# Kernel tuning notes

Measured on AMD Instinct MI355X. Metric: run time of the kernel, lower is better.

Reference implementation:

```python
import jax, jax.numpy as jnp
import numpy as np

DIM = 128
NUM_LAYERS = 2
N_LEGO = 50000
N_POINT = 100000
E_LL = 500000
E_PP = 400000
E_LP = 500000
E_PL = 500000


def _seg_softmax(score, seg, n):
    m = jax.ops.segment_max(score, seg, num_segments=n)
    m = jnp.where(jnp.isfinite(m), m, 0.0)
    e = jnp.exp(score - m[seg])
    d = jax.ops.segment_sum(e, seg, num_segments=n)
    return e / (d[seg] + 1e-16)


def _trans_conv(xs, xd, src, dst, Wq, bq, Wk, bk, Wv, bv, Ws, bs):
    # PyG TransformerConv, heads=1, root skip, no edge features
    q = xd @ Wq + bq
    k = xs @ Wk + bk
    v = xs @ Wv + bv
    score = (q[dst] * k[src]).sum(-1) / jnp.sqrt(jnp.asarray(DIM, q.dtype))
    a = _seg_softmax(score, dst, xd.shape[0])
    agg = jax.ops.segment_sum(a[:, None] * v[src], dst, num_segments=xd.shape[0])
    return agg + xd @ Ws + bs


def _gat_conv(xs, xd, src, dst, W, a_src, a_dst, b):
    # PyG GATConv, heads=1, add_self_loops=False, shared lin for src/dst
    hs = xs @ W
    hd = xd @ W
    score = jax.nn.leaky_relu((hs @ a_src)[src] + (hd @ a_dst)[dst], 0.2)
    a = _seg_softmax(score, dst, xd.shape[0])
    return jax.ops.segment_sum(a[:, None] * hs[src], dst, num_segments=xd.shape[0]) + b


def _edge_conv(x, src, dst, W1, b1, W2, b2):
    # PyG EdgeConv: max_j MLP([x_i, x_j - x_i]); BN treated as identity (eval)
    xi = x[dst]
    h = jax.nn.relu(jnp.concatenate([xi, x[src] - xi], axis=-1) @ W1 + b1)
    m = h @ W2 + b2
    agg = jax.ops.segment_max(m, dst, num_segments=x.shape[0])
    return jnp.where(jnp.isfinite(agg), agg, 0.0)


def _forward(x_lego, x_point, tWq, tbq, tWk, tbk, tWv, tbv, tWs, tbs,
             eW1, eb1, eW2, eb2, gW, gAs, gAd, gb,
             ll_src, ll_dst, pp_src, pp_dst, lp_src, lp_dst, pl_src, pl_dst):
    for layer in range(NUM_LAYERS):
        iA = 2 * layer        # first HeteroConv in the stack
        iB = 2 * layer + 1    # second HeteroConv
        i_lp = 2 * layer      # GAT lego->point instance
        i_pl = 2 * layer + 1  # GAT point->lego instance
        # conv A: 4 relations, HeteroConv sum-aggregation per dst type
        lego_a = _trans_conv(x_lego, x_lego, ll_src, ll_dst,
                             tWq[iA], tbq[iA], tWk[iA], tbk[iA], tWv[iA], tbv[iA], tWs[iA], tbs[iA]) \
               + _gat_conv(x_point, x_lego, pl_src, pl_dst, gW[i_pl], gAs[i_pl], gAd[i_pl], gb[i_pl])
        point_a = _edge_conv(x_point, pp_src, pp_dst, eW1[iA], eb1[iA], eW2[iA], eb2[iA]) \
                + _gat_conv(x_lego, x_point, lp_src, lp_dst, gW[i_lp], gAs[i_lp], gAd[i_lp], gb[i_lp])
        # conv B: intra-type relations only
        x_lego = _trans_conv(lego_a, lego_a, ll_src, ll_dst,
                             tWq[iB], tbq[iB], tWk[iB], tbk[iB], tWv[iB], tbv[iB], tWs[iB], tbs[iB])
        x_point = _edge_conv(point_a, pp_src, pp_dst, eW1[iB], eb1[iB], eW2[iB], eb2[iB])
    return x_lego, x_point


def setup_inputs() -> dict:
    key = jax.random.key(0)
    ks = jax.random.split(key, 32)
    NT = 2 * NUM_LAYERS  # conv instances per conv type
    s = np.float32(1.0 / np.sqrt(DIM))
    sh = np.float32(1.0 / np.sqrt(4 * DIM))
    return {
        "x_lego": jax.random.normal(ks[0], (N_LEGO, DIM), jnp.float32),
        "x_point": jax.random.normal(ks[1], (N_POINT, DIM), jnp.float32),
        "tWq": jax.random.normal(ks[2], (NT, DIM, DIM), jnp.float32) * s,
        "tbq": jnp.zeros((NT, DIM), jnp.float32),
        "tWk": jax.random.normal(ks[3], (NT, DIM, DIM), jnp.float32) * s,
        "tbk": jnp.zeros((NT, DIM), jnp.float32),
        "tWv": jax.random.normal(ks[4], (NT, DIM, DIM), jnp.float32) * s,
        "tbv": jnp.zeros((NT, DIM), jnp.float32),
        "tWs": jax.random.normal(ks[5], (NT, DIM, DIM), jnp.float32) * s,
        "tbs": jnp.zeros((NT, DIM), jnp.float32),
        "eW1": jax.random.normal(ks[6], (NT, 2 * DIM, 4 * DIM), jnp.float32) * s,
        "eb1": jnp.zeros((NT, 4 * DIM), jnp.float32),
        "eW2": jax.random.normal(ks[7], (NT, 4 * DIM, DIM), jnp.float32) * sh,
        "eb2": jnp.zeros((NT, DIM), jnp.float32),
        "gW": jax.random.normal(ks[8], (NT, DIM, DIM), jnp.float32) * s,
        "gAs": jax.random.normal(ks[9], (NT, DIM), jnp.float32) * s,
        "gAd": jax.random.normal(ks[10], (NT, DIM), jnp.float32) * s,
        "gb": jnp.zeros((NT, DIM), jnp.float32),
        "ll_src": jax.random.randint(ks[11], (E_LL,), 0, N_LEGO),
        "ll_dst": jax.random.randint(ks[12], (E_LL,), 0, N_LEGO),
        "pp_src": jax.random.randint(ks[13], (E_PP,), 0, N_POINT),
        "pp_dst": jax.random.randint(ks[14], (E_PP,), 0, N_POINT),
        "lp_src": jax.random.randint(ks[15], (E_LP,), 0, N_LEGO),
        "lp_dst": jax.random.randint(ks[16], (E_LP,), 0, N_POINT),
        "pl_src": jax.random.randint(ks[17], (E_PL,), 0, N_POINT),
        "pl_dst": jax.random.randint(ks[18], (E_PL,), 0, N_LEGO),
    }


def reference(x_lego, x_point, tWq, tbq, tWk, tbk, tWv, tbv, tWs, tbs,
              eW1, eb1, eW2, eb2, gW, gAs, gAd, gb,
              ll_src, ll_dst, pp_src, pp_dst, lp_src, lp_dst, pl_src, pl_dst):
    return _forward(x_lego, x_point, tWq, tbq, tWk, tbk, tWv, tbv, tWs, tbs,
                    eW1, eb1, eW2, eb2, gW, gAs, gAd, gb,
                    ll_src, ll_dst, pp_src, pp_dst, lp_src, lp_dst, pl_src, pl_dst)
```

## Files before the change

### kernel.cpp

```cpp
#include <hip/hip_runtime.h>


typedef unsigned int u32;
typedef unsigned short u16;

#define NL 50000
#define NP 100000
#define ELL 500000
#define EPPE 400000
#define ELPE 500000
#define EPLE 500000
#define ENC_NEG_INF 0x007FFFFFu

using bf16x8 = __attribute__((ext_vector_type(8))) short;
using f32x4  = __attribute__((ext_vector_type(4))) float;
using u16x4  = __attribute__((ext_vector_type(4))) unsigned short;

__device__ __forceinline__ float bf2f(u16 h) { return __uint_as_float(((u32)h) << 16); }
__device__ __forceinline__ u16 f2bf(float f) {
    u32 u = __float_as_uint(f);
    u += 0x7FFFu + ((u >> 16) & 1u);
    return (u16)(u >> 16);
}
__device__ __forceinline__ u32 encf(float f) {
    u32 u = __float_as_uint(f);
    return (u & 0x80000000u) ? ~u : (u | 0x80000000u);
}
__device__ __forceinline__ float decf(u32 u) {
    return __uint_as_float((u & 0x80000000u) ? (u ^ 0x80000000u) : ~u);
}

__global__ void k_detect(const u32* __restrict__ x, u32* __restrict__ flag) {
    int lane = threadIdx.x;
    u16 lo = (u16)(x[lane] & 0xFFFFu);
    float a = fabsf(bf2f(lo));
    int inband = (a > 1e-4f && a < 100.f) ? 1 : 0;
    unsigned long long m = __ballot(inband);
    if (lane == 0) flag[0] = (__popcll(m) >= 32) ? 1u : 0u;
}


__global__ __launch_bounds__(256) void k_cast_any(const void* __restrict__ in,
                                                  float* __restrict__ out, int n,
                                                  const u32* __restrict__ flag) {
    int i = blockIdx.x * 256 + threadIdx.x;
    if (i >= n) return;
    if (flag[0]) out[i] = bf2f(((const u16*)in)[i]);
    else         out[i] = ((const float*)in)[i];
}

__global__ __launch_bounds__(256) void k_store_out(const float* __restrict__ in,
                                                   void* __restrict__ out, size_t off, int n,
                                                   const u32* __restrict__ flag) {
    int i = blockIdx.x * 256 + threadIdx.x;
    if (i >= n) return;
    if (flag[0]) ((u16*)out)[off + i] = f2bf(in[i]);
    else         ((float*)out)[off + i] = in[i];
}

__global__ __launch_bounds__(256) void k_fill_u32(u32* __restrict__ p, u32 v, int n) {
    int i = blockIdx.x * 256 + threadIdx.x;
    if (i < n) p[i] = v;
}

__global__ void k_add128(const float* __restrict__ a, const float* __restrict__ b,
                         float* __restrict__ o) {
    int t = threadIdx.x;
    o[t] = a[t] + b[t];
}

__global__ __launch_bounds__(256) void k_tcast(const float* __restrict__ in,
                                               u16* __restrict__ out,
                                               int K, int N, int total) {
    int i = blockIdx.x * 256 + threadIdx.x;
    if (i >= total) return;
    int per = K * N;
    int c = i / per, r = i - c * per;
    int k = r / N, n = r - k * N;
    out[(size_t)c * per + (size_t)n * K + k] = f2bf(in[i]);
}

__global__ __launch_bounds__(256) void k_w1mod(float* __restrict__ w, int total) {
    int i = blockIdx.x * 256 + threadIdx.x;
    if (i >= total) return;
    int c = i >> 16;
    int r = (i >> 9) & 127;
    int col = i & 511;
    float* base = w + c * 131072;
    base[r * 512 + col] -= base[(r + 128) * 512 + col];
}

__global__ __launch_bounds__(256) void k_split(const float4* __restrict__ x,
                                               u16x4* __restrict__ xh,
                                               u16x4* __restrict__ xl, int n4) {
    int i = blockIdx.x * 256 + threadIdx.x;
    if (i >= n4) return;
    float4 f = x[i];
    float fv[4] = {f.x, f.y, f.z, f.w};
    u16x4 h, l;
#pragma unroll
    for (int j = 0; j < 4; ++j) {
        u16 hi = f2bf(fv[j]);
        h[j] = hi;
        l[j] = f2bf(fv[j] - bf2f(hi));
    }
    xh[i] = h; xl[i] = l;
}

__global__ void k_matvec2(const float* __restrict__ W, const float* __restrict__ a0,
                          const float* __restrict__ a1, float* __restrict__ o) {
    __shared__ float as[128];
    const float* a = blockIdx.x ? a1 : a0;
    int t = threadIdx.x;
    as[t] = a[t];
    __syncthreads();
    float s = 0.f;
#pragma unroll 8
    for (int i = 0; i < 128; ++i) s += W[t * 128 + i] * as[i];
    o[blockIdx.x * 128 + t] = s;
}

__global__ __launch_bounds__(256) void k_node_scalar(const float* __restrict__ X,
                                                     const float* __restrict__ wv,
                                                     float* __restrict__ s, int n) {
    int wid = (blockIdx.x * 256 + threadIdx.x) >> 6;
    int lane = threadIdx.x & 63;
    if (wid >= n) return;
    const float* xr = X + (size_t)wid * 128;
    float v = xr[lane] * wv[lane] + xr[lane + 64] * wv[lane + 64];
#pragma unroll
    for (int o = 32; o; o >>= 1) v += __shfl_xor(v, o);
    if (lane == 0) s[wid] = v;
}


__global__ __launch_bounds__(256) void k_deg(const int* __restrict__ dst,
                                             int* __restrict__ deg, int E) {
    int i = blockIdx.x * 256 + threadIdx.x;
    if (i < E) atomicAdd(deg + dst[i], 1);
}

__global__ __launch_bounds__(256) void k_scan1(const int* __restrict__ deg,
                                               int* __restrict__ rp,
                                               int* __restrict__ aux, int n) {
    __shared__ int ls[256];
    int t = threadIdx.x;
    int i = blockIdx.x * 256 + t;
    int v = (i < n) ? deg[i] : 0;
    ls[t] = v;
    __syncthreads();
#pragma unroll
    for (int off = 1; off < 256; off <<= 1) {
        int a = (t >= off) ? ls[t - off] : 0;
        __syncthreads();
        ls[t] += a;
        __syncthreads();
    }
    if (i < n) rp[i] = ls[t] - v;
    if (t == 255) aux[blockIdx.x] = ls[255];
}

__global__ __launch_bounds__(512) void k_scan2(int* __restrict__ aux, int nb) {
    __shared__ int ls[512];
    int t = threadIdx.x;
    int v = (t < nb) ? aux[t] : 0;
    ls[t] = v;
    __syncthreads();
#pragma unroll
    for (int off = 1; off < 512; off <<= 1) {
        int a = (t >= off) ? ls[t - off] : 0;
        __syncthreads();
        ls[t] += a;
        __syncthreads();
    }
    if (t < nb) aux[t] = ls[t] - v;
}

__global__ __launch_bounds__(256) void k_scan3(int* __restrict__ rp,
                                               const int* __restrict__ aux,
                                               int n, int E) {
    int i = blockIdx.x * 256 + threadIdx.x;
    if (i > n) return;
    if (i == n) rp[n] = E;
    else        rp[i] += aux[i >> 8];
}

__global__ __launch_bounds__(256) void k_copy_i32(const int* __restrict__ a,
                                                  int* __restrict__ b, int n) {
    int i = blockIdx.x * 256 + threadIdx.x;
    if (i < n) b[i] = a[i];
}

__global__ __launch_bounds__(256) void k_scat(const int* __restrict__ src,
                                              const int* __restrict__ dst,
                                              int* __restrict__ cur,
                                              int* __restrict__ col, int E) {
    int i = blockIdx.x * 256 + threadIdx.x;
    if (i >= E) return;
    int pos = atomicAdd(cur + dst[i], 1);
    col[pos] = src[i];
}


__global__ __launch_bounds__(256) void k_attn_trans(const float* __restrict__ Tq,
                                                    const float* __restrict__ Tk,
                                                    const float* __restrict__ Tv,
                                                    const int* __restrict__ rp,
                                                    const int* __restrict__ col,
                                                    float* __restrict__ out, int nd) {
    int row = (blockIdx.x * 256 + threadIdx.x) >> 6;
    int lane = threadIdx.x & 63;
    if (row >= nd) return;
    int e0 = rp[row], e1 = rp[row + 1];
    if (e0 >= e1) return;
    const float* q = Tq + (size_t)row * 128;
    float q0 = q[lane], q1 = q[lane + 64];
    float m = -3.0e38f, l = 0.f, o0 = 0.f, o1 = 0.f;
    for (int e = e0; e < e1; ++e) {
        int s = col[e];
        const float* kr = Tk + (size_t)s * 128;
        float d = q0 * kr[lane] + q1 * kr[lane + 64];
#pragma unroll
        for (int off = 32; off; off >>= 1) d += __shfl_xor(d, off);
        d *= 0.08838834764831845f;
        float mn = fmaxf(m, d);
        float al = expf(m - mn);
        float p  = expf(d - mn);
        const float* vr = Tv + (size_t)s * 128;
        l  = l * al + p;
        o0 = o0 * al + p * vr[lane];
        o1 = o1 * al + p * vr[lane + 64];
        m = mn;
    }
    float inv = 1.f / (l + 1e-16f);
    size_t base = (size_t)row * 128;
    out[base + lane]      += o0 * inv;
    out[base + lane + 64] += o1 * inv;
}

__global__ __launch_bounds__(256) void k_attn_gat(const float* __restrict__ hs,
                                                  const float* __restrict__ ss,
                                                  const float* __restrict__ sd,
                                                  const int* __restrict__ rp,
                                                  const int* __restrict__ col,
                                                  float* __restrict__ out, int nd) {
    int row = (blockIdx.x * 256 + threadIdx.x) >> 6;
    int lane = threadIdx.x & 63;
    if (row >= nd) return;
    int e0 = rp[row], e1 = rp[row + 1];
    if (e0 >= e1) return;
    float sdv = sd[row];
    float m = -3.0e38f, l = 0.f, o0 = 0.f, o1 = 0.f;
    for (int e = e0; e < e1; ++e) {
        int s = col[e];
        float sc = ss[s] + sdv;
        sc = sc > 0.f ? sc : 0.2f * sc;
        float mn = fmaxf(m, sc);
        float al = expf(m - mn);
        float p  = expf(sc - mn);
        const float* hr = hs + (size_t)s * 128;
        l  = l * al + p;
        o0 = o0 * al + p * hr[lane];
        o1 = o1 * al + p * hr[lane + 64];
        m = mn;
    }
    float inv = 1.f / (l + 1e-16f);
    size_t base = (size_t)row * 128;
    out[base + lane]      += o0 * inv;
    out[base + lane + 64] += o1 * inv;
}

#define LSTR 40

__global__ __launch_bounds__(256) void k_mgemm(const float* __restrict__ A_,
                                               const u16* __restrict__ Wt,
                                               const float* __restrict__ bias,
                                               float* __restrict__ Cout,
                                               int M, int N, int K) {
    __shared__ u16 Ahs[128 * LSTR];
    __shared__ u16 Als[128 * LSTR];
    __shared__ u16 Bss[128 * LSTR];
    const int tid = threadIdx.x;
    const int m0 = blockIdx.y * 128, n0 = blockIdx.x * 128;

    const int srow = tid >> 1, sseg = (tid & 1) * 16;
    int arow = m0 + srow;
    if (arow >= M) arow = M - 1;
    const float* Af = A_ + (size_t)arow * K + sseg;
    u16* AhW = &Ahs[srow * LSTR + sseg];
    u16* AlW = &Als[srow * LSTR + sseg];
    const u16* Bp = Wt + (size_t)(n0 + srow) * K + sseg;
    u16* BsW = &Bss[srow * LSTR + sseg];

    const int lane = tid & 63, wv = tid >> 6;
    const int mw = (wv >> 1) * 64, nw = (wv & 1) * 64;
    const int fm = lane & 15, fq = lane >> 4;
    const u16* aRh = &Ahs[(mw + fm) * LSTR + fq * 8];
    const u16* aRl = &Als[(mw + fm) * LSTR + fq * 8];
    const u16* bR  = &Bss[(nw + fm) * LSTR + fq * 8];

    f32x4 acc[4][4];
#pragma unroll
    for (int i = 0; i < 4; ++i)
#pragma unroll
        for (int j = 0; j < 4; ++j) { acc[i][j][0]=0.f; acc[i][j][1]=0.f; acc[i][j][2]=0.f; acc[i][j][3]=0.f; }

    for (int k0 = 0; k0 < K; k0 += 32) {
        __syncthreads();
        float4 f0 = *(const float4*)(Af + k0);
        float4 f1 = *(const float4*)(Af + k0 + 4);
        float4 f2 = *(const float4*)(Af + k0 + 8);
        float4 f3 = *(const float4*)(Af + k0 + 12);
        float v[16] = {f0.x,f0.y,f0.z,f0.w, f1.x,f1.y,f1.z,f1.w,
                       f2.x,f2.y,f2.z,f2.w, f3.x,f3.y,f3.z,f3.w};
        u32 hp[8], lp[8];
#pragma unroll
        for (int i = 0; i < 8; ++i) {
            float x0 = v[2 * i], x1 = v[2 * i + 1];
            u16 h0 = f2bf(x0), h1 = f2bf(x1);
            u16 l0 = f2bf(x0 - bf2f(h0)), l1 = f2bf(x1 - bf2f(h1));
            hp[i] = (u32)h0 | ((u32)h1 << 16);
            lp[i] = (u32)l0 | ((u32)l1 << 16);
        }
        uint4 h04 = {hp[0], hp[1], hp[2], hp[3]}, h48 = {hp[4], hp[5], hp[6], hp[7]};
        uint4 l04 = {lp[0], lp[1], lp[2], lp[3]}, l48 = {lp[4], lp[5], lp[6], lp[7]};
        *(uint4*)AhW = h04; *(uint4*)(AhW + 8) = h48;
        *(uint4*)AlW = l04; *(uint4*)(AlW + 8) = l48;
        *(uint4*)BsW       = *(const uint4*)(Bp + k0);
        *(uint4*)(BsW + 8) = *(const uint4*)(Bp + k0 + 8);
        __syncthreads();

        bf16x8 ah[4], al[4], bfr[4];
#pragma unroll
        for (int i = 0; i < 4; ++i) ah[i]  = *(const bf16x8*)(aRh + i * 16 * LSTR);
#pragma unroll
        for (int i = 0; i < 4; ++i) al[i]  = *(const bf16x8*)(aRl + i * 16 * LSTR);
#pragma unroll
        for (int j = 0; j < 4; ++j) bfr[j] = *(const bf16x8*)(bR + j * 16 * LSTR);
#pragma unroll
        for (int i = 0; i < 4; ++i)
#pragma unroll
            for (int j = 0; j < 4; ++j) {
                acc[i][j] = __builtin_amdgcn_mfma_f32_16x16x32_bf16(ah[i], bfr[j],
                                                                    acc[i][j], 0, 0, 0);
                acc[i][j] = __builtin_amdgcn_mfma_f32_16x16x32_bf16(al[i], bfr[j],
                                                                    acc[i][j], 0, 0, 0);
            }
    }

    float bb[4];
#pragma unroll
    for (int j = 0; j < 4; ++j)
        bb[j] = bias ? bias[n0 + nw + j * 16 + fm] : 0.f;
#pragma unroll
    for (int i = 0; i < 4; ++i) {
#pragma unroll
        for (int reg = 0; reg < 4; ++reg) {
            int r = m0 + mw + i * 16 + fq * 4 + reg;
            if (r >= M) continue;
#pragma unroll
            for (int j = 0; j < 4; ++j)
                Cout[(size_t)r * N + n0 + nw + j * 16 + fm] = acc[i][j][reg] + bb[j];
        }
    }
}

#define LSTRH 72

__global__ __launch_bounds__(256) void k_edge_fused(const u16* __restrict__ Xh,
                                                    const u16* __restrict__ Xl,
                                                    const int* __restrict__ esrc,
                                                    const int* __restrict__ edst,
                                                    const u16* __restrict__ W1t,
                                                    const float* __restrict__ b1,
                                                    const u16* __restrict__ W2t,
                                                    u32* __restrict__ agg, int E) {
    __shared__ u16 Ahs[128 * LSTR];
    __shared__ u16 Als[128 * LSTR];
    __shared__ u16 Bss[128 * LSTR];
    __shared__ u16 Hhs[128 * LSTRH];
    __shared__ u16 Hls[128 * LSTRH];
    const int tid = threadIdx.x;
    const int e0 = blockIdx.x * 128;

    const int srow = tid >> 1, sseg = (tid & 1) * 16;
    int er = e0 + srow;
    if (er >= E) er = E - 1;
    const u16* xsh = Xh + (size_t)esrc[er] * 128;
    const u16* xsl = Xl + (size_t)esrc[er] * 128;
    const u16* xdh = Xh + (size_t)edst[er] * 128;
    const u16* xdl = Xl + (size_t)edst[er] * 128;
    u16* AhW = &Ahs[srow * LSTR + sseg];
    u16* AlW = &Als[srow * LSTR + sseg];

    const int lane = tid & 63, wv = tid >> 6;
    const int fm = lane & 15, fq = lane >> 4;
    const int mw1 = (wv >> 1) * 64, nw1 = (wv & 1) * 32;
    const int mw2 = (wv >> 1) * 64, nw2 = (wv & 1) * 64;
    const u16* aRh1 = &Ahs[(mw1 + fm) * LSTR + fq * 8];
    const u16* aRl1 = &Als[(mw1 + fm) * LSTR + fq * 8];
    const u16* bR1  = &Bss[(nw1 + fm) * LSTR + fq * 8];
    const u16* aRh2 = &Hhs[(mw2 + fm) * LSTRH + fq * 8];
    const u16* aRl2 = &Hls[(mw2 + fm) * LSTRH + fq * 8];
    const u16* bR2  = &Bss[(nw2 + fm) * LSTR + fq * 8];

    f32x4 macc[4][4];
#pragma unroll
    for (int i = 0; i < 4; ++i)
#pragma unroll
        for (int j = 0; j < 4; ++j) { macc[i][j][0]=0.f; macc[i][j][1]=0.f; macc[i][j][2]=0.f; macc[i][j][3]=0.f; }

    for (int nc = 0; nc < 8; ++nc) {
        f32x4 hacc[4][2];
#pragma unroll
        for (int i = 0; i < 4; ++i)
#pragma unroll
            for (int j = 0; j < 2; ++j) { hacc[i][j][0]=0.f; hacc[i][j][1]=0.f; hacc[i][j][2]=0.f; hacc[i][j][3]=0.f; }

        for (int k0 = 0; k0 < 256; k0 += 32) {
            __syncthreads();
            int kk = k0 + sseg;
            const u16 *ph, *pl;
            if (kk < 128) { ph = xdh + kk;       pl = xdl + kk; }
            else          { ph = xsh + kk - 128; pl = xsl + kk - 128; }
            uint4 h04 = *(const uint4*)ph;
            uint4 h48 = *(const uint4*)(ph + 8);
            uint4 l04 = *(const uint4*)pl;
            uint4 l48 = *(const uint4*)(pl + 8);
            *(uint4*)AhW = h04; *(uint4*)(AhW + 8) = h48;
            *(uint4*)AlW = l04; *(uint4*)(AlW + 8) = l48;
            {
                int nrow = tid >> 2, kseg = (tid & 3) * 8;
                *(uint4*)&Bss[nrow * LSTR + kseg] =
                    *(const uint4*)(W1t + (size_t)(nc * 64 + nrow) * 256 + k0 + kseg);
            }
            __syncthreads();

            bf16x8 ah[4], al[4], bfr[2];
#pragma unroll
            for (int i = 0; i < 4; ++i) ah[i] = *(const bf16x8*)(aRh1 + i * 16 * LSTR);
#pragma unroll
            for (int i = 0; i < 4; ++i) al[i] = *(const bf16x8*)(aRl1 + i * 16 * LSTR);
#pragma unroll
            for (int j = 0; j < 2; ++j) bfr[j] = *(const bf16x8*)(bR1 + j * 16 * LSTR);
#pragma unroll
            for (int i = 0; i < 4; ++i)
#pragma unroll
                for (int j = 0; j < 2; ++j) {
                    hacc[i][j] = __builtin_amdgcn_mfma_f32_16x16x32_bf16(ah[i], bfr[j],
                                                                         hacc[i][j], 0, 0, 0);
                    hacc[i][j] = __builtin_amdgcn_mfma_f32_16x16x32_bf16(al[i], bfr[j],
                                                                         hacc[i][j], 0, 0, 0);
                }
        }
#pragma unroll
        for (int j = 0; j < 2; ++j) {
            int hk = nw1 + j * 16 + fm;
            float bb = b1[nc * 64 + hk];
#pragma unroll
            for (int i = 0; i < 4; ++i)
#pragma unroll
                for (int reg = 0; reg < 4; ++reg) {
                    int hr = mw1 + i * 16 + fq * 4 + reg;
                    float h = hacc[i][j][reg] + bb;
                    h = h > 0.f ? h : 0.f;
                    u16 hi = f2bf(h);
                    u16 lo = f2bf(h - bf2f(hi));
                    Hhs[hr * LSTRH + hk] = hi;
                    Hls[hr * LSTRH + hk] = lo;
                }
        }
        for (int k0 = 0; k0 < 64; k0 += 32) {
            __syncthreads();
            {
                int nrow = tid >> 1, kseg = (tid & 1) * 16;
                const u16* wp = W2t + (size_t)nrow * 512 + nc * 64 + k0 + kseg;
                *(uint4*)&Bss[nrow * LSTR + kseg]     = *(const uint4*)wp;
                *(uint4*)&Bss[nrow * LSTR + kseg + 8] = *(const uint4*)(wp + 8);
            }
            __syncthreads();

            bf16x8 ah[4], al[4], bfr[4];
#pragma unroll
            for (int i = 0; i < 4; ++i) ah[i] = *(const bf16x8*)(aRh2 + k0 + i * 16 * LSTRH);
#pragma unroll
            for (int i = 0; i < 4; ++i) al[i] = *(const bf16x8*)(aRl2 + k0 + i * 16 * LSTRH);
#pragma unroll
            for (int j = 0; j < 4; ++j) bfr[j] = *(const bf16x8*)(bR2 + j * 16 * LSTR);
#pragma unroll
            for (int i = 0; i < 4; ++i)
#pragma unroll
                for (int j = 0; j < 4; ++j) {
                    macc[i][j] = __builtin_amdgcn_mfma_f32_16x16x32_bf16(ah[i], bfr[j],
                                                                         macc[i][j], 0, 0, 0);
                    macc[i][j] = __builtin_amdgcn_mfma_f32_16x16x32_bf16(al[i], bfr[j],
                                                                         macc[i][j], 0, 0, 0);
                }
        }
        __syncthreads();
    }

#pragma unroll
    for (int i = 0; i < 4; ++i) {
#pragma unroll
        for (int reg = 0; reg < 4; ++reg) {
            int r = mw2 + i * 16 + fq * 4 + reg;
            int e = e0 + r;
            if (e >= E) continue;
            u32* base = agg + (size_t)edst[e] * 128 + nw2;
#pragma unroll
            for (int j = 0; j < 4; ++j)
                atomicMax(base + j * 16 + fm, encf(macc[i][j][reg]));
        }
    }
}

__global__ __launch_bounds__(256) void k_decode(u32* __restrict__ agg,
                                                const float* __restrict__ b2,
                                                const float* __restrict__ gb, int n) {
    int i = blockIdx.x * 256 + threadIdx.x;
    if (i >= n) return;
    int c = i & 127;
    u32 u = agg[i];
    float v = (u == ENC_NEG_INF) ? 0.f : (decf(u) + b2[c]);
    if (gb) v += gb[c];
    ((float*)agg)[i] = v;
}


extern "C" void kernel_launch(void* const* d_in, const int* in_sizes, int n_in,
                              void* d_out, int out_size, void* d_ws, size_t ws_size,
                              hipStream_t stream) {
    (void)in_sizes; (void)out_size;
    if (n_in < 26) return;
    if (ws_size < (size_t)240000000) return;

    const void* in_xl  = d_in[0];
    const void* in_xp  = d_in[1];
    const void* in_tWq = d_in[2];
    const void* in_tbq = d_in[3];
    const void* in_tWk = d_in[4];
    const void* in_tbk = d_in[5];
    const void* in_tWv = d_in[6];
    const void* in_tbv = d_in[7];
    const void* in_tWs = d_in[8];
    const void* in_tbs = d_in[9];
    const void* in_eW1 = d_in[10];
    const void* in_eb1 = d_in[11];
    const void* in_eW2 = d_in[12];
    const void* in_eb2 = d_in[13];
    const void* in_gW  = d_in[14];
    const void* in_gAs = d_in[15];
    const void* in_gAd = d_in[16];
    const void* in_gb  = d_in[17];
    const int* ll_src = (const int*)d_in[18];
    const int* ll_dst = (const int*)d_in[19];
    const int* pp_src = (const int*)d_in[20];
    const int* pp_dst = (const int*)d_in[21];
    const int* lp_src = (const int*)d_in[22];
    const int* lp_dst = (const int*)d_in[23];
    const int* pl_src = (const int*)d_in[24];
    const int* pl_dst = (const int*)d_in[25];

    char* w = (char*)d_ws;
    auto alloc = [&](size_t bytes) -> char* {
        char* p = w;
        w += (bytes + 255) & ~(size_t)255;
        return p;
    };
    float* XL   = (float*)alloc((size_t)NL * 128 * 4);
    float* XP   = (float*)alloc((size_t)NP * 128 * 4);
    float* LA   = (float*)alloc((size_t)NL * 128 * 4);
    float* PA   = (float*)alloc((size_t)NP * 128 * 4);
    float* ssrc = (float*)alloc((size_t)NP * 4);
    float* sdst = (float*)alloc((size_t)NP * 4);
    float* wv2  = (float*)alloc(256 * 4);
    float* comb = (float*)alloc(128 * 4);
    u32*  dflag = (u32*)  alloc(256);
    float* tbqf = (float*)alloc(512 * 4);
    float* tbkf = (float*)alloc(512 * 4);
    float* tbvf = (float*)alloc(512 * 4);
    float* tbsf = (float*)alloc(512 * 4);
    float* eb1f = (float*)alloc(2048 * 4);
    float* eb2f = (float*)alloc(512 * 4);
    float* gWf  = (float*)alloc(65536 * 4);
    float* gAsf = (float*)alloc(512 * 4);
    float* gAdf = (float*)alloc(512 * 4);
    float* gbf  = (float*)alloc(512 * 4);
    u16* tWqt = (u16*)alloc(65536 * 2);
    u16* tWkt = (u16*)alloc(65536 * 2);
    u16* tWvt = (u16*)alloc(65536 * 2);
    u16* tWst = (u16*)alloc(65536 * 2);
    u16* gWt  = (u16*)alloc(65536 * 2);
    u16* eW1t = (u16*)alloc(524288 * 2);
    u16* eW2t = (u16*)alloc(262144 * 2);
    int* rp_ll  = (int*)alloc((NL + 1) * 4);
    int* rp_lp  = (int*)alloc((NP + 1) * 4);
    int* rp_pl  = (int*)alloc((NL + 1) * 4);
    int* col_ll = (int*)alloc((size_t)ELL * 4);
    int* col_lp = (int*)alloc((size_t)ELPE * 4);
    int* col_pl = (int*)alloc((size_t)EPLE * 4);
    char* U = alloc(76800000);
    float* tWqf = (float*)U;
    float* tWkf = tWqf + 65536;
    float* tWvf = tWkf + 65536;
    float* tWsf = tWvf + 65536;
    float* eW1f = tWsf + 65536;
    float* eW2f = eW1f + 524288;
    float* Tq  = (float*)U;
    float* Tk  = Tq + (size_t)NL * 128;
    float* Tv  = Tk + (size_t)NL * 128;
    float* Ghs = (float*)U;
    u16* Xph = (u16*)U;
    u16* Xpl = Xph + (size_t)NP * 128;

    k_detect<<<1, 64, 0, stream>>>((const u32*)in_xl, dflag);

    auto cast = [&](const void* s_, float* d_, int n) {
        k_cast_any<<<(n + 255) / 256, 256, 0, stream>>>(s_, d_, n, dflag);
    };
    auto fillu = [&](void* p, u32 v, int n) {
        k_fill_u32<<<(n + 255) / 256, 256, 0, stream>>>((u32*)p, v, n);
    };
    auto tcast = [&](const float* s_, u16* d_, int K, int N, int nconv) {
        int total = nconv * K * N;
        k_tcast<<<(total + 255) / 256, 256, 0, stream>>>(s_, d_, K, N, total);
    };

    cast(in_xl, XL, NL * 128);
    cast(in_xp, XP, NP * 128);
    cast(in_tWq, tWqf, 65536); cast(in_tbq, tbqf, 512);
    cast(in_tWk, tWkf, 65536); cast(in_tbk, tbkf, 512);
    cast(in_tWv, tWvf, 65536); cast(in_tbv, tbvf, 512);
    cast(in_tWs, tWsf, 65536); cast(in_tbs, tbsf, 512);
    cast(in_eW1, eW1f, 524288); cast(in_eb1, eb1f, 2048);
    cast(in_eW2, eW2f, 262144); cast(in_eb2, eb2f, 512);
    cast(in_gW, gWf, 65536);
    cast(in_gAs, gAsf, 512); cast(in_gAd, gAdf, 512); cast(in_gb, gbf, 512);

    k_w1mod<<<(262144 + 255) / 256, 256, 0, stream>>>(eW1f, 262144);

    tcast(tWqf, tWqt, 128, 128, 4);
    tcast(tWkf, tWkt, 128, 128, 4);
    tcast(tWvf, tWvt, 128, 128, 4);
    tcast(tWsf, tWst, 128, 128, 4);
    tcast(gWf,  gWt,  128, 128, 4);
    tcast(eW1f, eW1t, 256, 512, 4);
    tcast(eW2f, eW2t, 512, 128, 4);

    int* deg = (int*)U;
    int* cur = deg + NP + 64;
    int* aux = cur + NP + 64;
    auto build_csr = [&](const int* src, const int* dst, int E, int nd,
                         int* rp, int* col) {
        int nb = (nd + 255) / 256;
        fillu(deg, 0u, nd);
        k_deg<<<(E + 255) / 256, 256, 0, stream>>>(dst, deg, E);
        k_scan1<<<nb, 256, 0, stream>>>(deg, rp, aux, nd);
        k_scan2<<<1, 512, 0, stream>>>(aux, nb);
        k_scan3<<<(nd + 256) / 256, 256, 0, stream>>>(rp, aux, nd, E);
        k_copy_i32<<<(nd + 255) / 256, 256, 0, stream>>>(rp, cur, nd);
        k_scat<<<(E + 255) / 256, 256, 0, stream>>>(src, dst, cur, col, E);
    };
    build_csr(ll_src, ll_dst, ELL, NL, rp_ll, col_ll);
    build_csr(lp_src, lp_dst, ELPE, NP, rp_lp, col_lp);
    build_csr(pl_src, pl_dst, EPLE, NL, rp_pl, col_pl);

    auto mgemm = [&](const float* A, const u16* Wt, const float* b, float* C,
                     int M, int N, int K) {
        dim3 g(N / 128, (M + 127) / 128);
        k_mgemm<<<g, 256, 0, stream>>>(A, Wt, b, C, M, N, K);
    };

    auto trans_agg = [&](const float* Xin, float* out, int conv) {
        mgemm(Xin, tWqt + conv * 16384, tbqf + conv * 128, Tq, NL, 128, 128);
        mgemm(Xin, tWkt + conv * 16384, tbkf + conv * 128, Tk, NL, 128, 128);
        mgemm(Xin, tWvt + conv * 16384, tbvf + conv * 128, Tv, NL, 128, 128);
        k_attn_trans<<<(NL + 3) / 4, 256, 0, stream>>>(Tq, Tk, Tv, rp_ll, col_ll,
                                                       out, NL);
    };
    auto gat_conv = [&](const float* Xs, int ns, int nd,
                        const float* Xd, const int* rp, const int* col,
                        int g, float* out) {
        k_matvec2<<<2, 128, 0, stream>>>(gWf + g * 16384, gAsf + g * 128,
                                         gAdf + g * 128, wv2);
        k_node_scalar<<<(ns * 64 + 255) / 256, 256, 0, stream>>>(Xs, wv2, ssrc, ns);
        k_node_scalar<<<(nd * 64 + 255) / 256, 256, 0, stream>>>(Xd, wv2 + 128, sdst, nd);
        mgemm(Xs, gWt + g * 16384, nullptr, Ghs, ns, 128, 128);
        k_attn_gat<<<(nd + 3) / 4, 256, 0, stream>>>(Ghs, ssrc, sdst, rp, col,
                                                     out, nd);
    };
    auto edge_conv = [&](const float* Xin, float* Xout, int conv, const float* gbext) {
        k_split<<<(NP * 32 + 255) / 256, 256, 0, stream>>>(
            (const float4*)Xin, (u16x4*)Xph, (u16x4*)Xpl, NP * 32);
        fillu(Xout, ENC_NEG_INF, NP * 128);
        k_edge_fused<<<(EPPE + 127) / 128, 256, 0, stream>>>(
            Xph, Xpl, pp_src, pp_dst,
            eW1t + conv * 131072, eb1f + conv * 512, eW2t + conv * 65536,
            (u32*)Xout, EPPE);
        k_decode<<<(NP * 128 + 255) / 256, 256, 0, stream>>>((u32*)Xout, eb2f + conv * 128,
                                                             gbext, NP * 128);
    };

    for (int layer = 0; layer < 2; ++layer) {
        int cA = 2 * layer, cB = cA + 1;
        int g_lp = 2 * layer, g_pl = 2 * layer + 1;

        k_add128<<<1, 128, 0, stream>>>(tbsf + cA * 128, gbf + g_pl * 128, comb);
        mgemm(XL, tWst + cA * 16384, comb, LA, NL, 128, 128);
        trans_agg(XL, LA, cA);
        gat_conv(XP, NP, NL, XL, rp_pl, col_pl, g_pl, LA);

        edge_conv(XP, PA, cA, gbf + g_lp * 128);
        gat_conv(XL, NL, NP, XP, rp_lp, col_lp, g_lp, PA);

        mgemm(LA, tWst + cB * 16384, tbsf + cB * 128, XL, NL, 128, 128);
        trans_agg(LA, XL, cB);
        edge_conv(PA, XP, cB, nullptr);
    }

    k_store_out<<<(NL * 128 + 255) / 256, 256, 0, stream>>>(XL, d_out, 0, NL * 128, dflag);
    k_store_out<<<(NP * 128 + 255) / 256, 256, 0, stream>>>(XP, d_out, (size_t)NL * 128,
                                                            NP * 128, dflag);
}
```

Measured before the change: 4.999 ms.

## Load EdgeConv MLP operands directly from global into MFMA fragments, dropping LDS staging

The fused EdgeConv kernel no longer stages gathered node features and weight tiles through shared memory. Each wave now reads its A fragments (x_dst / x_src hi/lo rows) and the W1/W2 B fragments straight from global memory into registers. The first GEMM is repartitioned so each wave owns 32 edges by 64 hidden columns instead of 64 by 32. This removes most LDS traffic and the per-k-step barriers, leaving only the hidden-tile exchange through LDS. In exchange, weight loads are repeated per wave from global/L2 instead of shared within the block, and the feature gathers are uncoalesced 16-byte loads whose latency is now exposed.

After: 5.578 ms. 1.12x slower.

```diff
diff --git a/kernel.cpp b/kernel.cpp
--- a/kernel.cpp
+++ b/kernel.cpp
@@ -375,34 +375,24 @@
                                                     const float* __restrict__ b1,
                                                     const u16* __restrict__ W2t,
                                                     u32* __restrict__ agg, int E) {
-    __shared__ u16 Ahs[128 * LSTR];
-    __shared__ u16 Als[128 * LSTR];
-    __shared__ u16 Bss[128 * LSTR];
     __shared__ u16 Hhs[128 * LSTRH];
     __shared__ u16 Hls[128 * LSTRH];
     const int tid = threadIdx.x;
     const int e0 = blockIdx.x * 128;
-
-    const int srow = tid >> 1, sseg = (tid & 1) * 16;
-    int er = e0 + srow;
-    if (er >= E) er = E - 1;
-    const u16* xsh = Xh + (size_t)esrc[er] * 128;
-    const u16* xsl = Xl + (size_t)esrc[er] * 128;
-    const u16* xdh = Xh + (size_t)edst[er] * 128;
-    const u16* xdl = Xl + (size_t)edst[er] * 128;
-    u16* AhW = &Ahs[srow * LSTR + sseg];
-    u16* AlW = &Als[srow * LSTR + sseg];
-
     const int lane = tid & 63, wv = tid >> 6;
     const int fm = lane & 15, fq = lane >> 4;
-    const int mw1 = (wv >> 1) * 64, nw1 = (wv & 1) * 32;
+    const int mw1 = wv * 32;
     const int mw2 = (wv >> 1) * 64, nw2 = (wv & 1) * 64;
-    const u16* aRh1 = &Ahs[(mw1 + fm) * LSTR + fq * 8];
-    const u16* aRl1 = &Als[(mw1 + fm) * LSTR + fq * 8];
-    const u16* bR1  = &Bss[(nw1 + fm) * LSTR + fq * 8];
-    const u16* aRh2 = &Hhs[(mw2 + fm) * LSTRH + fq * 8];
-    const u16* aRl2 = &Hls[(mw2 + fm) * LSTRH + fq * 8];
-    const u16* bR2  = &Bss[(nw2 + fm) * LSTR + fq * 8];
+
+    const u16 *p0h[2], *p0l[2], *p1h[2], *p1l[2];
+    {
+        int er0 = e0 + mw1 + fm;       if (er0 >= E) er0 = E - 1;
+        int er1 = e0 + mw1 + 16 + fm;  if (er1 >= E) er1 = E - 1;
+        size_t d0 = (size_t)edst[er0] * 128, s0 = (size_t)esrc[er0] * 128;
+        size_t d1 = (size_t)edst[er1] * 128, s1 = (size_t)esrc[er1] * 128;
+        p0h[0] = Xh + d0; p0l[0] = Xl + d0; p0h[1] = Xh + s0; p0l[1] = Xl + s0;
+        p1h[0] = Xh + d1; p1l[0] = Xl + d1; p1h[1] = Xh + s1; p1l[1] = Xl + s1;
+    }
 
     f32x4 macc[4][4];
 #pragma unroll
@@ -411,54 +401,54 @@
         for (int j = 0; j < 4; ++j) { macc[i][j][0]=0.f; macc[i][j][1]=0.f; macc[i][j][2]=0.f; macc[i][j][3]=0.f; }
 
     for (int nc = 0; nc < 8; ++nc) {
-        f32x4 hacc[4][2];
-#pragma unroll
-        for (int i = 0; i < 4; ++i)
-#pragma unroll
-            for (int j = 0; j < 2; ++j) { hacc[i][j][0]=0.f; hacc[i][j][1]=0.f; hacc[i][j][2]=0.f; hacc[i][j][3]=0.f; }
-
-        for (int k0 = 0; k0 < 256; k0 += 32) {
-            __syncthreads();
-            int kk = k0 + sseg;
-            const u16 *ph, *pl;
-            if (kk < 128) { ph = xdh + kk;       pl = xdl + kk; }
-            else          { ph = xsh + kk - 128; pl = xsl + kk - 128; }
-            uint4 h04 = *(const uint4*)ph;
-            uint4 h48 = *(const uint4*)(ph + 8);
-            uint4 l04 = *(const uint4*)pl;
-            uint4 l48 = *(const uint4*)(pl + 8);
-            *(uint4*)AhW = h04; *(uint4*)(AhW + 8) = h48;
-            *(uint4*)AlW = l04; *(uint4*)(AlW + 8) = l48;
-            {
-                int nrow = tid >> 2, kseg = (tid & 3) * 8;
-                *(uint4*)&Bss[nrow * LSTR + kseg] =
-                    *(const uint4*)(W1t + (size_t)(nc * 64 + nrow) * 256 + k0 + kseg);
+        f32x4 hacc[2][4];
+#pragma unroll
+        for (int i = 0; i < 2; ++i)
+#pragma unroll
+            for (int j = 0; j < 4; ++j) { hacc[i][j][0]=0.f; hacc[i][j][1]=0.f; hacc[i][j][2]=0.f; hacc[i][j][3]=0.f; }
+
+        const u16* wbase = W1t + (size_t)(nc * 64 + fm) * 256 + fq * 8;
+
+        auto s1step = [&](const u16* a0h, const u16* a0l, const u16* a1h,
+                          const u16* a1l, int kw, int ka) {
+            bf16x8 ah0 = *(const bf16x8*)(a0h + ka);
+            bf16x8 al0 = *(const bf16x8*)(a0l + ka);
+            bf16x8 ah1 = *(const bf16x8*)(a1h + ka);
+            bf16x8 al1 = *(const bf16x8*)(a1l + ka);
+            bf16x8 bfr[4];
+#pragma unroll
+            for (int j = 0; j < 4; ++j)
+                bfr[j] = *(const bf16x8*)(wbase + kw + j * 16 * 256);
+#pragma unroll
+            for (int j = 0; j < 4; ++j) {
+                hacc[0][j] = __builtin_amdgcn_mfma_f32_16x16x32_bf16(ah0, bfr[j],
+                                                                     hacc[0][j], 0, 0, 0);
+                hacc[0][j] = __builtin_amdgcn_mfma_f32_16x16x32_bf16(al0, bfr[j],
+                                                                     hacc[0][j], 0, 0, 0);
             }
-            __syncthreads();
-
-            bf16x8 ah[4], al[4], bfr[2];
-#pragma unroll
-            for (int i = 0; i < 4; ++i) ah[i] = *(const bf16x8*)(aRh1 + i * 16 * LSTR);
-#pragma unroll
-            for (int i = 0; i < 4; ++i) al[i] = *(const bf16x8*)(aRl1 + i * 16 * LSTR);
-#pragma unroll
-            for (int j = 0; j < 2; ++j) bfr[j] = *(const bf16x8*)(bR1 + j * 16 * LSTR);
-#pragma unroll
-            for (int i = 0; i < 4; ++i)
-#pragma unroll
-                for (int j = 0; j < 2; ++j) {
-                    hacc[i][j] = __builtin_amdgcn_mfma_f32_16x16x32_bf16(ah[i], bfr[j],
-                                                                         hacc[i][j], 0, 0, 0);
-                    hacc[i][j] = __builtin_amdgcn_mfma_f32_16x16x32_bf16(al[i], bfr[j],
-                                                                         hacc[i][j], 0, 0, 0);
-                }
-        }
-#pragma unroll
-        for (int j = 0; j < 2; ++j) {
-            int hk = nw1 + j * 16 + fm;
+#pragma unroll
+            for (int j = 0; j < 4; ++j) {
+                hacc[1][j] = __builtin_amdgcn_mfma_f32_16x16x32_bf16(ah1, bfr[j],
+                                                                     hacc[1][j], 0, 0, 0);
+                hacc[1][j] = __builtin_amdgcn_mfma_f32_16x16x32_bf16(al1, bfr[j],
+                                                                     hacc[1][j], 0, 0, 0);
+            }
+        };
+
+#pragma unroll 2
+        for (int k0 = 0; k0 < 128; k0 += 32)
+            s1step(p0h[0], p0l[0], p1h[0], p1l[0], k0, k0 + fq * 8);
+#pragma unroll 2
+        for (int k0 = 128; k0 < 256; k0 += 32)
+            s1step(p0h[1], p0l[1], p1h[1], p1l[1], k0, k0 - 128 + fq * 8);
+
+        __syncthreads();
+#pragma unroll
+        for (int j = 0; j < 4; ++j) {
+            int hk = j * 16 + fm;
             float bb = b1[nc * 64 + hk];
 #pragma unroll
-            for (int i = 0; i < 4; ++i)
+            for (int i = 0; i < 2; ++i)
 #pragma unroll
                 for (int reg = 0; reg < 4; ++reg) {
                     int hr = mw1 + i * 16 + fq * 4 + reg;
@@ -470,23 +460,21 @@
                     Hls[hr * LSTRH + hk] = lo;
                 }
         }
+        __syncthreads();
+
+        const u16* w2base = W2t + (size_t)(nw2 + fm) * 512 + nc * 64 + fq * 8;
+#pragma unroll
         for (int k0 = 0; k0 < 64; k0 += 32) {
-            __syncthreads();
-            {
-                int nrow = tid >> 1, kseg = (tid & 1) * 16;
-                const u16* wp = W2t + (size_t)nrow * 512 + nc * 64 + k0 + kseg;
-                *(uint4*)&Bss[nrow * LSTR + kseg]     = *(const uint4*)wp;
-                *(uint4*)&Bss[nrow * LSTR + kseg + 8] = *(const uint4*)(wp + 8);
+            bf16x8 ah[4], al[4], bfr[4];
+#pragma unroll
+            for (int i = 0; i < 4; ++i) {
+                int off = (mw2 + i * 16 + fm) * LSTRH + k0 + fq * 8;
+                ah[i] = *(const bf16x8*)&Hhs[off];
+                al[i] = *(const bf16x8*)&Hls[off];
             }
-            __syncthreads();
-
-            bf16x8 ah[4], al[4], bfr[4];
-#pragma unroll
-            for (int i = 0; i < 4; ++i) ah[i] = *(const bf16x8*)(aRh2 + k0 + i * 16 * LSTRH);
-#pragma unroll
-            for (int i = 0; i < 4; ++i) al[i] = *(const bf16x8*)(aRl2 + k0 + i * 16 * LSTRH);
-#pragma unroll
-            for (int j = 0; j < 4; ++j) bfr[j] = *(const bf16x8*)(bR2 + j * 16 * LSTR);
+#pragma unroll
+            for (int j = 0; j < 4; ++j)
+                bfr[j] = *(const bf16x8*)(w2base + k0 + j * 16 * 512);
 #pragma unroll
             for (int i = 0; i < 4; ++i)
 #pragma unroll
@@ -497,7 +485,6 @@
                                                                          macc[i][j], 0, 0, 0);
                 }
         }
-        __syncthreads();
     }
 
 #pragma unroll
```
